# Kernel tuning notes

Hardware: AMD Instinct MI355X
Metric: run time of the kernel (lower is better)

Reference implementation:

```python
import jax, jax.numpy as jnp
import numpy as np

B, L, H, A = 2, 384, 256, 14  # batch, total residues (binder+target), hidden, atoms/residue


def setup_inputs() -> dict:
    key = jax.random.key(0)
    ks = jax.random.split(key, 8)
    s = 1.0 / np.sqrt(H)
    h = jax.random.normal(ks[0], (B, L, H), jnp.float32)          # encoder output
    X = jax.random.normal(ks[1], (B, L, A, 3), jnp.float32)       # coordinates
    mask = jnp.ones((B, L), jnp.int32)                             # residue validity mask
    Wx_w = jax.random.normal(ks[2], (H, H), jnp.float32) * s
    Wx_b = jnp.zeros((H,), jnp.float32)
    Ux_w = jax.random.normal(ks[3], (H, H), jnp.float32) * s
    Ux_b = jnp.zeros((H,), jnp.float32)
    Tx_w = jax.random.normal(ks[4], (A, H), jnp.float32) * s
    Tx_b = jnp.zeros((A,), jnp.float32)
    return dict(h=h, X=X, mask=mask, Wx_w=Wx_w, Wx_b=Wx_b,
                Ux_w=Ux_w, Ux_b=Ux_b, Tx_w=Tx_w, Tx_b=Tx_b)


def reference(h, X, mask, Wx_w, Wx_b, Ux_w, Ux_b, Tx_w, Tx_b):
    # One recurrent coordinate-update step of FADocker._forward.
    m = mask.astype(h.dtype)                                   # (B, L)
    hw = h @ Wx_w.T + Wx_b                                     # (B, L, H)  = W_x(h)
    hu = h @ Ux_w.T + Ux_b                                     # (B, L, H)  = U_x(h)
    mij = hw[:, :, None, :] + hu[:, None, :, :]                # (B, L, L, H)
    gate = jnp.einsum('bijh,ah->bija', jax.nn.relu(mij), Tx_w) + Tx_b  # (B, L, L, A) = T_x(mij)
    xij = (X[:, :, None] - X[:, None, :]) * gate[..., None]   # (B, L, L, A, 3)
    f = jnp.einsum('bijac,bj->biac', xij, m)                   # masked sum over j
    f = f / (1e-6 + m.sum(axis=1)[:, None, None, None])        # (B, L, A, 3)
    return X + jnp.clip(f, -20.0, 20.0)
```

## Files before the change

kernel.cpp:

```cpp
#include <hip/hip_runtime.h>
#include <hip/hip_bf16.h>

#define HDIM 256
#define LDIM 384
#define BDIM 2
#define ADIM 14
#define H2 (HDIM / 2)

typedef __attribute__((ext_vector_type(8))) short bf16x8;
typedef __attribute__((ext_vector_type(4))) float f32x4;

static __device__ __forceinline__ unsigned pack_bf16(float x, float y) {
    __hip_bfloat162 t = __float22bfloat162_rn(make_float2(x, y));
    return *reinterpret_cast<unsigned*>(&t);
}

static __device__ __forceinline__ bf16x8 cvt8(float4 a, float4 b) {
    union { unsigned u[4]; bf16x8 v; } r;
    r.u[0] = pack_bf16(a.x, a.y); r.u[1] = pack_bf16(a.z, a.w);
    r.u[2] = pack_bf16(b.x, b.y); r.u[3] = pack_bf16(b.z, b.w);
    return r.v;
}

__global__ __launch_bounds__(64) void k_gemm(
    const float* __restrict__ h,
    const float* __restrict__ Wx_w, const float* __restrict__ Wx_b,
    const float* __restrict__ Ux_w, const float* __restrict__ Ux_b,
    float* __restrict__ hw, unsigned* __restrict__ huP)
{
    const int lane = threadIdx.x;
    const int n = lane & 15;
    const int quad = lane >> 4;

    const int c0   = blockIdx.x * 32;
    const int row0 = blockIdx.y * 32;

    const float* __restrict__ wbase = (c0 < HDIM) ? &Wx_w[c0 * HDIM]
                                                  : &Ux_w[(c0 - HDIM) * HDIM];
    const float* __restrict__ wl0 = wbase + (n) * HDIM + quad * 8;
    const float* __restrict__ wl1 = wbase + (16 + n) * HDIM + quad * 8;
    const float* __restrict__ hl0 = h + (row0 + n) * HDIM + quad * 8;
    const float* __restrict__ hl1 = h + (row0 + 16 + n) * HDIM + quad * 8;

    f32x4 acc00 = {0,0,0,0}, acc01 = {0,0,0,0}, acc10 = {0,0,0,0}, acc11 = {0,0,0,0};

    #pragma unroll 4
    for (int kc = 0; kc < 8; ++kc) {
        const int ko = kc * 32;
        const bf16x8 a0 = cvt8(*(const float4*)(wl0 + ko), *(const float4*)(wl0 + ko + 4));
        const bf16x8 a1 = cvt8(*(const float4*)(wl1 + ko), *(const float4*)(wl1 + ko + 4));
        const bf16x8 b0 = cvt8(*(const float4*)(hl0 + ko), *(const float4*)(hl0 + ko + 4));
        const bf16x8 b1 = cvt8(*(const float4*)(hl1 + ko), *(const float4*)(hl1 + ko + 4));
        acc00 = __builtin_amdgcn_mfma_f32_16x16x32_bf16(a0, b0, acc00, 0, 0, 0);
        acc01 = __builtin_amdgcn_mfma_f32_16x16x32_bf16(a0, b1, acc01, 0, 0, 0);
        acc10 = __builtin_amdgcn_mfma_f32_16x16x32_bf16(a1, b0, acc10, 0, 0, 0);
        acc11 = __builtin_amdgcn_mfma_f32_16x16x32_bf16(a1, b1, acc11, 0, 0, 0);
    }

    const int grow0 = row0 + n;
    const int grow1 = row0 + 16 + n;
    const int b = row0 / LDIM;
    const int i0 = grow0 - b * LDIM, i1 = grow1 - b * LDIM;

    if (c0 < HDIM) {
        #pragma unroll
        for (int ct = 0; ct < 2; ++ct) {
            const int cb = c0 + ct * 16 + quad * 4;
            const float4 bias = *(const float4*)&Wx_b[cb];
            const f32x4 aR0 = ct ? acc10 : acc00;
            const f32x4 aR1 = ct ? acc11 : acc01;
            *(float4*)&hw[grow0 * HDIM + cb] =
                make_float4(aR0[0] + bias.x, aR0[1] + bias.y, aR0[2] + bias.z, aR0[3] + bias.w);
            *(float4*)&hw[grow1 * HDIM + cb] =
                make_float4(aR1[0] + bias.x, aR1[1] + bias.y, aR1[2] + bias.z, aR1[3] + bias.w);
        }
    } else {
        unsigned* __restrict__ hub = &huP[b * H2 * LDIM];
        #pragma unroll
        for (int ct = 0; ct < 2; ++ct) {
            const int ch = (c0 - HDIM) + ct * 16 + quad * 4;
            const float4 bias = *(const float4*)&Ux_b[ch];
            const f32x4 aR0 = ct ? acc10 : acc00;
            const f32x4 aR1 = ct ? acc11 : acc01;
            const int h2 = ch >> 1;
            hub[(h2)     * LDIM + i0] = pack_bf16(aR0[0] + bias.x, aR0[1] + bias.y);
            hub[(h2 + 1) * LDIM + i0] = pack_bf16(aR0[2] + bias.z, aR0[3] + bias.w);
            hub[(h2)     * LDIM + i1] = pack_bf16(aR1[0] + bias.x, aR1[1] + bias.y);
            hub[(h2 + 1) * LDIM + i1] = pack_bf16(aR1[2] + bias.z, aR1[3] + bias.w);
        }
    }
}

__global__ __launch_bounds__(384) void k_main(
    const float* __restrict__ hw, const unsigned* __restrict__ huP,
    const float* __restrict__ X, const int* __restrict__ mask,
    const float* __restrict__ Tx_w, const float* __restrict__ Tx_b,
    float* __restrict__ out)
{
    __shared__ unsigned TxP[16 * 130];
    __shared__ float m_lds[LDIM];
    __shared__ float part2[24 * 16 * 4];
    __shared__ float part_m[24];

    const int i = blockIdx.x, b = blockIdx.y;
    const int tid = threadIdx.x;
    const int w = tid >> 6;
    const int lane = tid & 63;
    const int n = lane & 15;
    const int quad = lane >> 4;

    for (int idx = tid; idx < 16 * 128; idx += 384) {
        const int nn = idx >> 7, k2 = idx & 127;
        unsigned v = 0;
        if (nn < ADIM) {
            const float2 tw = *(const float2*)&Tx_w[nn * HDIM + 2 * k2];
            v = pack_bf16(tw.x, tw.y);
        }
        TxP[nn * 130 + k2] = v;
    }
    m_lds[tid] = (float)mask[b * LDIM + tid];
    __syncthreads();

    const float* __restrict__ hwrow = &hw[(b * LDIM + i) * HDIM];
    const unsigned* __restrict__ hub = &huP[b * H2 * LDIM];

    f32x4 acc[4];
    #pragma unroll
    for (int t = 0; t < 4; ++t) acc[t] = (f32x4){0.f, 0.f, 0.f, 0.f};

    const int jbase = w * 64 + n;

    #pragma unroll 2
    for (int kc = 0; kc < 8; ++kc) {
        union { unsigned u[4]; bf16x8 v; } bu;
        const int bofs = n * 130 + kc * 16 + quad * 4;
        *(uint2*)&bu.u[0] = *(const uint2*)&TxP[bofs];
        *(uint2*)&bu.u[2] = *(const uint2*)&TxP[bofs + 2];
        const float4 hwa = *(const float4*)(hwrow + kc * 32 + quad * 8);
        const float4 hwb = *(const float4*)(hwrow + kc * 32 + quad * 8 + 4);
        const float hv[8] = {hwa.x, hwa.y, hwa.z, hwa.w, hwb.x, hwb.y, hwb.z, hwb.w};
        const int h2base = kc * 16 + quad * 4;
        #pragma unroll
        for (int t = 0; t < 4; ++t) {
            const unsigned* __restrict__ hp = &hub[h2base * LDIM + jbase + t * 16];
            union { unsigned u[4]; bf16x8 v; } au;
            #pragma unroll
            for (int d = 0; d < 4; ++d) {
                const unsigned pk = hp[d * LDIM];
                const float lo = __uint_as_float(pk << 16);
                const float hi = __uint_as_float(pk & 0xffff0000u);
                const float t0 = fmaxf(hv[2 * d] + lo, 0.f);
                const float t1 = fmaxf(hv[2 * d + 1] + hi, 0.f);
                au.u[d] = pack_bf16(t0, t1);
            }
            acc[t] = __builtin_amdgcn_mfma_f32_16x16x32_bf16(au.v, bu.v, acc[t], 0, 0, 0);
        }
    }

    float s1 = 0.f, s2x = 0.f, s2y = 0.f, s2z = 0.f, pm = 0.f;
    if (n < ADIM) {
        const float txb = Tx_b[n];
        #pragma unroll
        for (int t = 0; t < 4; ++t) {
            #pragma unroll
            for (int r = 0; r < 4; ++r) {
                const int jd = (w * 4 + t) * 16 + quad * 4 + r;
                const float m = m_lds[jd];
                const float g = acc[t][r] + txb;
                const float mg = m * g;
                const float* __restrict__ Xp = &X[((b * LDIM + jd) * ADIM + n) * 3];
                s1 += mg;
                s2x = fmaf(mg, Xp[0], s2x);
                s2y = fmaf(mg, Xp[1], s2y);
                s2z = fmaf(mg, Xp[2], s2z);
                pm += m;
            }
        }
    }
    {
        f32x4 sv = {s2x, s2y, s2z, s1};
        *(f32x4*)&part2[((w * 4 + quad) * 16 + n) * 4] = sv;
    }
    if (n == 0) part_m[w * 4 + quad] = pm;
    __syncthreads();

    if (tid < 42) {
        const int a = tid / 3, c = tid % 3;
        float S2 = 0.f, S1 = 0.f, msum = 0.f;
        #pragma unroll 4
        for (int g = 0; g < 24; ++g) {
            const float* __restrict__ p = &part2[(g * 16 + a) * 4];
            S2 += p[c]; S1 += p[3]; msum += part_m[g];
        }
        const float denom = 1e-6f + msum;
        const int idx = ((b * LDIM + i) * ADIM + a) * 3 + c;
        const float xi = X[idx];
        float f = (xi * S1 - S2) / denom;
        f = fminf(fmaxf(f, -20.f), 20.f);
        out[idx] = xi + f;
    }
}

extern "C" void kernel_launch(void* const* d_in, const int* in_sizes, int n_in,
                              void* d_out, int out_size, void* d_ws, size_t ws_size,
                              hipStream_t stream) {
    (void)in_sizes; (void)n_in; (void)out_size; (void)ws_size;
    const float* h    = (const float*)d_in[0];
    const float* X    = (const float*)d_in[1];
    const int*   mask = (const int*)  d_in[2];
    const float* Wx_w = (const float*)d_in[3];
    const float* Wx_b = (const float*)d_in[4];
    const float* Ux_w = (const float*)d_in[5];
    const float* Ux_b = (const float*)d_in[6];
    const float* Tx_w = (const float*)d_in[7];
    const float* Tx_b = (const float*)d_in[8];
    float* out = (float*)d_out;

    float*    hw  = (float*)d_ws;
    unsigned* huP = (unsigned*)(hw + BDIM * LDIM * HDIM);

    k_gemm<<<dim3(16, 24), dim3(64), 0, stream>>>(h, Wx_w, Wx_b, Ux_w, Ux_b, hw, huP);
    k_main<<<dim3(LDIM, BDIM), 384, 0, stream>>>(hw, huP, X, mask, Tx_w, Tx_b, out);
}
```

Baseline: 92.47 us.

## Stage hu tiles through LDS with register prefetch and row-major hu layout

```diff
diff --git a/kernel.cpp b/kernel.cpp
--- a/kernel.cpp
+++ b/kernel.cpp
@@ -75,7 +75,7 @@
                 make_float4(aR1[0] + bias.x, aR1[1] + bias.y, aR1[2] + bias.z, aR1[3] + bias.w);
         }
     } else {
-        unsigned* __restrict__ hub = &huP[b * H2 * LDIM];
+        unsigned* __restrict__ hub = &huP[b * LDIM * H2];
         #pragma unroll
         for (int ct = 0; ct < 2; ++ct) {
             const int ch = (c0 - HDIM) + ct * 16 + quad * 4;
@@ -83,21 +83,24 @@
             const f32x4 aR0 = ct ? acc10 : acc00;
             const f32x4 aR1 = ct ? acc11 : acc01;
             const int h2 = ch >> 1;
-            hub[(h2)     * LDIM + i0] = pack_bf16(aR0[0] + bias.x, aR0[1] + bias.y);
-            hub[(h2 + 1) * LDIM + i0] = pack_bf16(aR0[2] + bias.z, aR0[3] + bias.w);
-            hub[(h2)     * LDIM + i1] = pack_bf16(aR1[0] + bias.x, aR1[1] + bias.y);
-            hub[(h2 + 1) * LDIM + i1] = pack_bf16(aR1[2] + bias.z, aR1[3] + bias.w);
-        }
-    }
-}
-
-__global__ __launch_bounds__(384) void k_main(
+            *(uint2*)&hub[i0 * H2 + h2] = make_uint2(
+                pack_bf16(aR0[0] + bias.x, aR0[1] + bias.y),
+                pack_bf16(aR0[2] + bias.z, aR0[3] + bias.w));
+            *(uint2*)&hub[i1 * H2 + h2] = make_uint2(
+                pack_bf16(aR1[0] + bias.x, aR1[1] + bias.y),
+                pack_bf16(aR1[2] + bias.z, aR1[3] + bias.w));
+        }
+    }
+}
+
+__global__ __launch_bounds__(384, 5) void k_main(
     const float* __restrict__ hw, const unsigned* __restrict__ huP,
     const float* __restrict__ X, const int* __restrict__ mask,
     const float* __restrict__ Tx_w, const float* __restrict__ Tx_b,
     float* __restrict__ out)
 {
     __shared__ unsigned TxP[16 * 130];
+    __shared__ __align__(16) unsigned hu_s[LDIM * 16];
     __shared__ float m_lds[LDIM];
     __shared__ float part2[24 * 16 * 4];
     __shared__ float part_m[24];
@@ -109,6 +112,15 @@
     const int n = lane & 15;
     const int quad = lane >> 4;
 
+    const unsigned* __restrict__ hub = &huP[b * LDIM * H2];
+
+    uint4 st[4];
+    #pragma unroll
+    for (int q = 0; q < 4; ++q) {
+        const int c = tid + q * 384;
+        st[q] = *(const uint4*)&hub[(c >> 2) * H2 + (c & 3) * 4];
+    }
+
     for (int idx = tid; idx < 16 * 128; idx += 384) {
         const int nn = idx >> 7, k2 = idx & 127;
         unsigned v = 0;
@@ -119,19 +131,30 @@
         TxP[nn * 130 + k2] = v;
     }
     m_lds[tid] = (float)mask[b * LDIM + tid];
+
+    #pragma unroll
+    for (int q = 0; q < 4; ++q) {
+        const int c = tid + q * 384;
+        *(uint4*)&hu_s[c * 4] = st[q];
+    }
     __syncthreads();
 
     const float* __restrict__ hwrow = &hw[(b * LDIM + i) * HDIM];
-    const unsigned* __restrict__ hub = &huP[b * H2 * LDIM];
 
     f32x4 acc[4];
     #pragma unroll
     for (int t = 0; t < 4; ++t) acc[t] = (f32x4){0.f, 0.f, 0.f, 0.f};
 
-    const int jbase = w * 64 + n;
-
-    #pragma unroll 2
+    #pragma unroll
     for (int kc = 0; kc < 8; ++kc) {
+        if (kc < 7) {
+            #pragma unroll
+            for (int q = 0; q < 4; ++q) {
+                const int c = tid + q * 384;
+                st[q] = *(const uint4*)&hub[(c >> 2) * H2 + (kc + 1) * 16 + (c & 3) * 4];
+            }
+        }
+
         union { unsigned u[4]; bf16x8 v; } bu;
         const int bofs = n * 130 + kc * 16 + quad * 4;
         *(uint2*)&bu.u[0] = *(const uint2*)&TxP[bofs];
@@ -139,14 +162,15 @@
         const float4 hwa = *(const float4*)(hwrow + kc * 32 + quad * 8);
         const float4 hwb = *(const float4*)(hwrow + kc * 32 + quad * 8 + 4);
         const float hv[8] = {hwa.x, hwa.y, hwa.z, hwa.w, hwb.x, hwb.y, hwb.z, hwb.w};
-        const int h2base = kc * 16 + quad * 4;
+
         #pragma unroll
         for (int t = 0; t < 4; ++t) {
-            const unsigned* __restrict__ hp = &hub[h2base * LDIM + jbase + t * 16];
+            union { uint4 q; unsigned u[4]; } ar;
+            ar.q = *(const uint4*)&hu_s[((w * 64 + t * 16 + n) * 16 + quad * 4)];
             union { unsigned u[4]; bf16x8 v; } au;
             #pragma unroll
             for (int d = 0; d < 4; ++d) {
-                const unsigned pk = hp[d * LDIM];
+                const unsigned pk = ar.u[d];
                 const float lo = __uint_as_float(pk << 16);
                 const float hi = __uint_as_float(pk & 0xffff0000u);
                 const float t0 = fmaxf(hv[2 * d] + lo, 0.f);
@@ -154,6 +178,16 @@
                 au.u[d] = pack_bf16(t0, t1);
             }
             acc[t] = __builtin_amdgcn_mfma_f32_16x16x32_bf16(au.v, bu.v, acc[t], 0, 0, 0);
+        }
+
+        __syncthreads();
+        if (kc < 7) {
+            #pragma unroll
+            for (int q = 0; q < 4; ++q) {
+                const int c = tid + q * 384;
+                *(uint4*)&hu_s[c * 4] = st[q];
+            }
+            __syncthreads();
         }
     }
 
```

Measured after the change: 124.7 us. 34.8% more time.

## Process two query rows per block to reuse hu loads and Tx fragments

Applied to the files above, without the earlier changes.

```diff
diff --git a/kernel.cpp b/kernel.cpp
--- a/kernel.cpp
+++ b/kernel.cpp
@@ -99,10 +99,10 @@
 {
     __shared__ unsigned TxP[16 * 130];
     __shared__ float m_lds[LDIM];
-    __shared__ float part2[24 * 16 * 4];
+    __shared__ float part2[2][24 * 16 * 4];
     __shared__ float part_m[24];
 
-    const int i = blockIdx.x, b = blockIdx.y;
+    const int i0 = blockIdx.x * 2, b = blockIdx.y;
     const int tid = threadIdx.x;
     const int w = tid >> 6;
     const int lane = tid & 63;
@@ -121,12 +121,16 @@
     m_lds[tid] = (float)mask[b * LDIM + tid];
     __syncthreads();
 
-    const float* __restrict__ hwrow = &hw[(b * LDIM + i) * HDIM];
+    const float* __restrict__ hwrow0 = &hw[(b * LDIM + i0) * HDIM];
+    const float* __restrict__ hwrow1 = hwrow0 + HDIM;
     const unsigned* __restrict__ hub = &huP[b * H2 * LDIM];
 
-    f32x4 acc[4];
+    f32x4 acc0[4], acc1[4];
     #pragma unroll
-    for (int t = 0; t < 4; ++t) acc[t] = (f32x4){0.f, 0.f, 0.f, 0.f};
+    for (int t = 0; t < 4; ++t) {
+        acc0[t] = (f32x4){0.f, 0.f, 0.f, 0.f};
+        acc1[t] = (f32x4){0.f, 0.f, 0.f, 0.f};
+    }
 
     const int jbase = w * 64 + n;
 
@@ -136,28 +140,34 @@
         const int bofs = n * 130 + kc * 16 + quad * 4;
         *(uint2*)&bu.u[0] = *(const uint2*)&TxP[bofs];
         *(uint2*)&bu.u[2] = *(const uint2*)&TxP[bofs + 2];
-        const float4 hwa = *(const float4*)(hwrow + kc * 32 + quad * 8);
-        const float4 hwb = *(const float4*)(hwrow + kc * 32 + quad * 8 + 4);
-        const float hv[8] = {hwa.x, hwa.y, hwa.z, hwa.w, hwb.x, hwb.y, hwb.z, hwb.w};
+        const float4 h0a = *(const float4*)(hwrow0 + kc * 32 + quad * 8);
+        const float4 h0b = *(const float4*)(hwrow0 + kc * 32 + quad * 8 + 4);
+        const float4 h1a = *(const float4*)(hwrow1 + kc * 32 + quad * 8);
+        const float4 h1b = *(const float4*)(hwrow1 + kc * 32 + quad * 8 + 4);
+        const float hv0[8] = {h0a.x, h0a.y, h0a.z, h0a.w, h0b.x, h0b.y, h0b.z, h0b.w};
+        const float hv1[8] = {h1a.x, h1a.y, h1a.z, h1a.w, h1b.x, h1b.y, h1b.z, h1b.w};
         const int h2base = kc * 16 + quad * 4;
         #pragma unroll
         for (int t = 0; t < 4; ++t) {
             const unsigned* __restrict__ hp = &hub[h2base * LDIM + jbase + t * 16];
-            union { unsigned u[4]; bf16x8 v; } au;
+            union { unsigned u[4]; bf16x8 v; } au0, au1;
             #pragma unroll
             for (int d = 0; d < 4; ++d) {
                 const unsigned pk = hp[d * LDIM];
                 const float lo = __uint_as_float(pk << 16);
                 const float hi = __uint_as_float(pk & 0xffff0000u);
-                const float t0 = fmaxf(hv[2 * d] + lo, 0.f);
-                const float t1 = fmaxf(hv[2 * d + 1] + hi, 0.f);
-                au.u[d] = pack_bf16(t0, t1);
+                au0.u[d] = pack_bf16(fmaxf(hv0[2 * d] + lo, 0.f),
+                                     fmaxf(hv0[2 * d + 1] + hi, 0.f));
+                au1.u[d] = pack_bf16(fmaxf(hv1[2 * d] + lo, 0.f),
+                                     fmaxf(hv1[2 * d + 1] + hi, 0.f));
             }
-            acc[t] = __builtin_amdgcn_mfma_f32_16x16x32_bf16(au.v, bu.v, acc[t], 0, 0, 0);
-        }
-    }
-
-    float s1 = 0.f, s2x = 0.f, s2y = 0.f, s2z = 0.f, pm = 0.f;
+            acc0[t] = __builtin_amdgcn_mfma_f32_16x16x32_bf16(au0.v, bu.v, acc0[t], 0, 0, 0);
+            acc1[t] = __builtin_amdgcn_mfma_f32_16x16x32_bf16(au1.v, bu.v, acc1[t], 0, 0, 0);
+        }
+    }
+
+    float s1A = 0.f, s2xA = 0.f, s2yA = 0.f, s2zA = 0.f;
+    float s1B = 0.f, s2xB = 0.f, s2yB = 0.f, s2zB = 0.f, pm = 0.f;
     if (n < ADIM) {
         const float txb = Tx_b[n];
         #pragma unroll
@@ -166,34 +176,42 @@
             for (int r = 0; r < 4; ++r) {
                 const int jd = (w * 4 + t) * 16 + quad * 4 + r;
                 const float m = m_lds[jd];
-                const float g = acc[t][r] + txb;
-                const float mg = m * g;
                 const float* __restrict__ Xp = &X[((b * LDIM + jd) * ADIM + n) * 3];
-                s1 += mg;
-                s2x = fmaf(mg, Xp[0], s2x);
-                s2y = fmaf(mg, Xp[1], s2y);
-                s2z = fmaf(mg, Xp[2], s2z);
+                const float x0 = Xp[0], x1 = Xp[1], x2 = Xp[2];
+                const float mg0 = m * (acc0[t][r] + txb);
+                s1A += mg0;
+                s2xA = fmaf(mg0, x0, s2xA);
+                s2yA = fmaf(mg0, x1, s2yA);
+                s2zA = fmaf(mg0, x2, s2zA);
+                const float mg1 = m * (acc1[t][r] + txb);
+                s1B += mg1;
+                s2xB = fmaf(mg1, x0, s2xB);
+                s2yB = fmaf(mg1, x1, s2yB);
+                s2zB = fmaf(mg1, x2, s2zB);
                 pm += m;
             }
         }
     }
     {
-        f32x4 sv = {s2x, s2y, s2z, s1};
-        *(f32x4*)&part2[((w * 4 + quad) * 16 + n) * 4] = sv;
+        const int po = ((w * 4 + quad) * 16 + n) * 4;
+        *(f32x4*)&part2[0][po] = (f32x4){s2xA, s2yA, s2zA, s1A};
+        *(f32x4*)&part2[1][po] = (f32x4){s2xB, s2yB, s2zB, s1B};
     }
     if (n == 0) part_m[w * 4 + quad] = pm;
     __syncthreads();
 
-    if (tid < 42) {
-        const int a = tid / 3, c = tid % 3;
+    if (tid < 84) {
+        const int ii = (tid >= 42) ? 1 : 0;
+        const int r  = tid - ii * 42;
+        const int a = r / 3, c = r % 3;
         float S2 = 0.f, S1 = 0.f, msum = 0.f;
         #pragma unroll 4
         for (int g = 0; g < 24; ++g) {
-            const float* __restrict__ p = &part2[(g * 16 + a) * 4];
+            const float* __restrict__ p = &part2[ii][(g * 16 + a) * 4];
             S2 += p[c]; S1 += p[3]; msum += part_m[g];
         }
         const float denom = 1e-6f + msum;
-        const int idx = ((b * LDIM + i) * ADIM + a) * 3 + c;
+        const int idx = ((b * LDIM + i0 + ii) * ADIM + a) * 3 + c;
         const float xi = X[idx];
         float f = (xi * S1 - S2) / denom;
         f = fminf(fmaxf(f, -20.f), 20.f);
@@ -220,5 +238,5 @@
     unsigned* huP = (unsigned*)(hw + BDIM * LDIM * HDIM);
 
     k_gemm<<<dim3(16, 24), dim3(64), 0, stream>>>(h, Wx_w, Wx_b, Ux_w, Ux_b, hw, huP);
-    k_main<<<dim3(LDIM, BDIM), 384, 0, stream>>>(hw, huP, X, mask, Tx_w, Tx_b, out);
-}
+    k_main<<<dim3(LDIM / 2, BDIM), 384, 0, stream>>>(hw, huP, X, mask, Tx_w, Tx_b, out);
+}
```

Result: slower. 94.90 us (+2.6%).
